# Kernel optimization log

Measured on AMD Instinct MI355X. Metric: run time of the kernel, lower is better.

The kernel has to match this reference:

```python
import jax, jax.numpy as jnp
import numpy as np

B, L, D, DFF, H, DK = 256, 193, 64, 256, 2, 32
EPS = 1e-5


def _ln(x, g, b):
    m = x.mean(-1, keepdims=True)
    v = ((x - m) ** 2).mean(-1, keepdims=True)
    return (x - m) / jnp.sqrt(v + EPS) * g + b


def setup_inputs() -> dict:
    key = jax.random.key(0)
    ks = jax.random.split(key, 20)
    inp = {}
    inp["state"] = jax.random.normal(ks[0], (B, L, D), jnp.float32)
    for i in range(6):
        inp[f"C{i+1}"] = jax.random.normal(ks[1 + i], (B, L, DFF), jnp.float32)
    s = 0.02
    # state Q/K/V projections (stored as [in, out]; y = x @ W + b)
    inp["Wq"] = jax.random.normal(ks[7], (D, D), jnp.float32) * s
    inp["Wk"] = jax.random.normal(ks[8], (D, D), jnp.float32) * s
    inp["Wv"] = jax.random.normal(ks[9], (D, D), jnp.float32) * s
    inp["bq"] = jnp.zeros((D,), jnp.float32)
    inp["bk"] = jnp.zeros((D,), jnp.float32)
    inp["bv"] = jnp.zeros((D,), jnp.float32)
    # context (C_cat, 6*dff=1536 -> 64) projections
    inp["WCq"] = jax.random.normal(ks[10], (6 * DFF, D), jnp.float32) * s
    inp["WCk"] = jax.random.normal(ks[11], (6 * DFF, D), jnp.float32) * s
    inp["WCv"] = jax.random.normal(ks[12], (6 * DFF, D), jnp.float32) * s
    inp["bCq"] = jnp.zeros((D,), jnp.float32)
    inp["bCk"] = jnp.zeros((D,), jnp.float32)
    inp["bCv"] = jnp.zeros((D,), jnp.float32)
    # LayerNorm params (6 QKV branch norms + norm1)
    for nm in ("QE", "KE", "VE", "QH", "KH", "VH", "1"):
        inp[f"g{nm}"] = jnp.ones((D,), jnp.float32)
        inp[f"be{nm}"] = jnp.zeros((D,), jnp.float32)
    # FFN
    inp["W1"] = jax.random.normal(ks[13], (D, 4 * D), jnp.float32) * s
    inp["bl1"] = jnp.zeros((4 * D,), jnp.float32)
    inp["W2"] = jax.random.normal(ks[14], (4 * D, D), jnp.float32) * s
    inp["bl2"] = jnp.zeros((D,), jnp.float32)
    return inp


def reference(state, C1, C2, C3, C4, C5, C6,
              Wq, Wk, Wv, bq, bk, bv,
              WCq, WCk, WCv, bCq, bCk, bCv,
              gQE, beQE, gKE, beKE, gVE, beVE,
              gQH, beQH, gKH, beKH, gVH, beVH,
              g1, be1, W1, bl1, W2, bl2):
    Ccat = jnp.concatenate([C1, C2, C3, C4, C5, C6], axis=-1)  # [B, L, 6*dff]
    # gated Q/K/V: LN(state proj) * LN(context proj)
    q = _ln(state @ Wq + bq, gQE, beQE) * _ln(Ccat @ WCq + bCq, gQH, beQH)
    k = _ln(state @ Wk + bk, gKE, beKE) * _ln(Ccat @ WCk + bCk, gKH, beKH)
    v = _ln(state @ Wv + bv, gVE, beVE) * _ln(Ccat @ WCv + bCv, gVH, beVH)
    q = q.reshape(B, L, H, DK).transpose(0, 2, 1, 3)  # [B, H, L, dk]
    k = k.reshape(B, L, H, DK).transpose(0, 2, 1, 3)
    v = v.reshape(B, L, H, DK).transpose(0, 2, 1, 3)
    scores = jnp.einsum("bhqd,bhkd->bhqk", q, k) / jnp.sqrt(jnp.float32(DK))
    attn = jax.nn.softmax(scores, axis=-1)
    out = jnp.einsum("bhqk,bhkd->bhqd", attn, v)
    attn_values = out.transpose(0, 2, 1, 3).reshape(B, L, H * DK)
    # dropout is identity in eval mode
    Z1 = state + attn_values
    Z2 = _ln(Z1, g1, be1)
    Z3 = jax.nn.gelu(Z2 @ W1 + bl1, approximate=False)
    Z4 = Z3 @ W2 + bl2
    Z5 = state + attn_values + Z4
    return Z5
```

## Files before the change

kernel.cpp:

```cpp
#include <hip/hip_runtime.h>
#include <math.h>

typedef unsigned short ushort_t;
typedef __attribute__((ext_vector_type(8))) short short8;
typedef __attribute__((ext_vector_type(4))) float floatx4;
typedef __attribute__((ext_vector_type(8))) unsigned short ushortx8;

#define NROW 49408
#define MT   772

__device__ __forceinline__ float b2f(ushort_t u){
  union { float f; unsigned int i; } v; v.i = ((unsigned int)u) << 16; return v.f;
}
__device__ __forceinline__ ushort_t f2b(float f){
  unsigned int i = __float_as_uint(f);
  unsigned int r = (i + 0x7FFFu + ((i >> 16) & 1u)) >> 16;
  return (ushort_t)r;
}

struct Args {
  const float *state,*C0,*C1,*C2,*C3,*C4,*C5;
  const float *Wq,*Wk,*Wv,*bq,*bk,*bv;
  const float *WCq,*WCk,*WCv,*bCq,*bCk,*bCv;
  const float *gQE,*beQE,*gKE,*beKE,*gVE,*beVE;
  const float *gQH,*beQH,*gKH,*beKH,*gVH,*beVH;
  const float *g1,*be1,*W1,*bl1,*W2,*bl2;
  float *qws,*kws,*vws;
  ushort_t *attws;
  ushort_t *weT,*whT,*w1T,*w2T;
  float *out;
};

__global__ __launch_bounds__(256) void k_prep(Args A){
  int i = blockIdx.x*256 + threadIdx.x;
  int stride = gridDim.x*256;
  const float* We[3] = {A.Wq, A.Wk, A.Wv};
  const float* Wh[3] = {A.WCq, A.WCk, A.WCv};
  for (int p=i; p<2*6144; p+=stride){
    int kc = p / 6144, r = p - kc*6144, n = r >> 5, kk = r & 31;
    A.weT[p] = f2b(We[n>>6][(kc*32+kk)*64 + (n&63)]);
  }
  for (int p=i; p<48*6144; p+=stride){
    int kc = p / 6144, r = p - kc*6144, n = r >> 5, kk = r & 31;
    A.whT[p] = f2b(Wh[n>>6][(kc*32+kk)*64 + (n&63)]);
  }
  for (int p=i; p<256*64; p+=stride){ int n=p>>6, k=p&63; A.w1T[p] = f2b(A.W1[k*256 + n]); }
  for (int p=i; p<64*256; p+=stride){ int n=p>>8, k=p&255; A.w2T[p] = f2b(A.W2[k*64 + n]); }
}

#define LDA 72
__global__ __launch_bounds__(256,2) void k_proj(Args A){
  const int mb = blockIdx.x;
  const int t  = threadIdx.x;
  const int w  = t >> 6;
  const int l  = t & 63;
  const int lr = l & 15;
  const int lq = l >> 4;
  const int arow = t >> 2, aseg = t & 3;

  struct __align__(16) SM {
    union {
      ushort_t Abuf[2][64*LDA];
      struct { float E[64][65]; float Hh[64][65]; } ln;
    };
  };
  __shared__ SM sm;

  floatx4 accH[3][4];
  floatx4 accE[3][4];
  #pragma unroll
  for (int jj=0;jj<3;jj++)
    #pragma unroll
    for (int ra=0;ra<4;ra++){ accH[jj][ra] = floatx4{0.f,0.f,0.f,0.f}; accE[jj][ra] = floatx4{0.f,0.f,0.f,0.f}; }

  auto loadA = [&](int k, float4* f){
    const float* src;
    if (k < 24){
      int sel = k >> 2;
      const float* cb = A.C0;
      if (sel==1) cb=A.C1; else if (sel==2) cb=A.C2; else if (sel==3) cb=A.C3;
      else if (sel==4) cb=A.C4; else if (sel==5) cb=A.C5;
      src = cb + (size_t)(mb*64 + arow)*256 + (k&3)*64 + aseg*16;
    } else {
      src = A.state + (size_t)(mb*64 + arow)*64 + aseg*16;
    }
    f[0] = ((const float4*)src)[0];
    f[1] = ((const float4*)src)[1];
    f[2] = ((const float4*)src)[2];
    f[3] = ((const float4*)src)[3];
  };
  auto loadB = [&](int k, short8* b){
    const ushort_t* bp = (k < 24) ? (A.whT + (size_t)(2*k)*6144) : A.weT;
    #pragma unroll
    for (int ks=0; ks<2; ++ks)
      #pragma unroll
      for (int jj=0; jj<3; ++jj)
        b[ks*3+jj] = *(const short8*)(bp + ks*6144 + (48*w + 16*jj + lr)*32 + lq*8);
  };
  auto storeA = [&](int buf, const float4* f){
    ushortx8 u0, u1;
    u0[0]=f2b(f[0].x); u0[1]=f2b(f[0].y); u0[2]=f2b(f[0].z); u0[3]=f2b(f[0].w);
    u0[4]=f2b(f[1].x); u0[5]=f2b(f[1].y); u0[6]=f2b(f[1].z); u0[7]=f2b(f[1].w);
    u1[0]=f2b(f[2].x); u1[1]=f2b(f[2].y); u1[2]=f2b(f[2].z); u1[3]=f2b(f[2].w);
    u1[4]=f2b(f[3].x); u1[5]=f2b(f[3].y); u1[6]=f2b(f[3].z); u1[7]=f2b(f[3].w);
    ushort_t* p = sm.Abuf[buf] + arow*LDA + aseg*16;
    *(ushortx8*)p = u0;
    *(ushortx8*)(p+8) = u1;
  };
  auto mfmaStep = [&](int cur, const short8* b, floatx4 (&acc)[3][4]){
    #pragma unroll
    for (int ks=0; ks<2; ++ks){
      short8 a[4];
      #pragma unroll
      for (int ra=0;ra<4;ra++)
        a[ra] = *(const short8*)(sm.Abuf[cur] + (16*ra + lr)*LDA + ks*32 + lq*8);
      #pragma unroll
      for (int jj=0;jj<3;jj++)
        #pragma unroll
        for (int ra=0;ra<4;ra++)
          acc[jj][ra] = __builtin_amdgcn_mfma_f32_16x16x32_bf16(a[ra], b[ks*3+jj], acc[jj][ra], 0,0,0);
    }
  };

  float4 rA[4], rB[4];
  short8 bA[6], bB[6];

  loadB(0, bA);
  loadA(0, rB);
  loadA(1, rA);
  storeA(0, rB);
  __syncthreads();

  for (int kc = 0; kc < 24; kc += 2){
    loadB(kc+1, bB);
    loadA(kc+2, rB);
    mfmaStep(0, bA, accH);
    storeA(1, rA);
    asm volatile("s_waitcnt lgkmcnt(0)" ::: "memory");
    __builtin_amdgcn_s_barrier();
    __builtin_amdgcn_sched_barrier(0);
    loadB(kc+2, bA);
    if (kc+3 <= 24) loadA(kc+3, rA);
    mfmaStep(1, bB, accH);
    storeA(0, rB);
    asm volatile("s_waitcnt lgkmcnt(0)" ::: "memory");
    __builtin_amdgcn_s_barrier();
    __builtin_amdgcn_sched_barrier(0);
  }
  mfmaStep(0, bA, accE);
  __syncthreads();

  const float* bEs[3]  = {A.bq,  A.bk,  A.bv};
  const float* bHs[3]  = {A.bCq, A.bCk, A.bCv};
  const float* gEs[3]  = {A.gQE, A.gKE, A.gVE};
  const float* beEs[3] = {A.beQE,A.beKE,A.beVE};
  const float* gHs[3]  = {A.gQH, A.gKH, A.gVH};
  const float* beHs[3] = {A.beQH,A.beKH,A.beVH};
  float* outw[3] = {A.qws, A.kws, A.vws};

  for (int g=0; g<3; ++g){
    #pragma unroll
    for (int jj=0;jj<3;jj++){
      int jg = 3*w + jj;
      if ((jg >> 2) == g){
        int colL = (jg & 3)*16 + lr;
        float be_ = bEs[g][colL];
        float bh_ = bHs[g][colL];
        #pragma unroll
        for (int ra=0;ra<4;ra++)
          #pragma unroll
          for (int r=0;r<4;r++){
            int row = 16*ra + lq*4 + r;
            sm.ln.E[row][colL]  = accE[jj][ra][r] + be_;
            sm.ln.Hh[row][colL] = accH[jj][ra][r] + bh_;
          }
      }
    }
    __syncthreads();
    {
      int r = t >> 2, q4 = t & 3;
      float sE=0.f, ssE=0.f, sH=0.f, ssH=0.f;
      #pragma unroll
      for (int c=0;c<16;c++){
        float e = sm.ln.E[r][q4*16+c];  sE += e; ssE += e*e;
        float h = sm.ln.Hh[r][q4*16+c]; sH += h; ssH += h*h;
      }
      sE  += __shfl_xor(sE,1);  sE  += __shfl_xor(sE,2);
      ssE += __shfl_xor(ssE,1); ssE += __shfl_xor(ssE,2);
      sH  += __shfl_xor(sH,1);  sH  += __shfl_xor(sH,2);
      ssH += __shfl_xor(ssH,1); ssH += __shfl_xor(ssH,2);
      float mE = sE*(1.f/64.f), vE = fmaxf(ssE*(1.f/64.f) - mE*mE, 0.f);
      float mH = sH*(1.f/64.f), vH = fmaxf(ssH*(1.f/64.f) - mH*mH, 0.f);
      float rE = rsqrtf(vE + 1e-5f), rH = rsqrtf(vH + 1e-5f);
      int G  = mb*64 + r;
      int bb = G / 193, lp = G - bb*193;
      float* ow = outw[g];
      #pragma unroll
      for (int c=0;c<16;c++){
        int cc = q4*16 + c;
        float e = (sm.ln.E[r][cc]-mE)*rE*gEs[g][cc] + beEs[g][cc];
        float h = (sm.ln.Hh[r][cc]-mH)*rH*gHs[g][cc] + beHs[g][cc];
        int hd = cc >> 5, d = cc & 31;
        ow[((size_t)(bb*2+hd)*193 + lp)*32 + d] = e*h;
      }
    }
    __syncthreads();
  }
}

__global__ __launch_bounds__(256) void k_attn(Args A){
  const int b = blockIdx.x, h = blockIdx.y;
  const int t = threadIdx.x;
  const size_t base = ((size_t)(b*2+h))*193*32;
  const float* __restrict__ kws = A.kws;
  const float* __restrict__ vws = A.vws;

  const int qrow = (t < 193) ? t : 192;
  float qreg[32], acc[32];
  {
    const float* qp = A.qws + base + qrow*32;
    #pragma unroll
    for (int d=0; d<32; d++){ qreg[d] = qp[d]; acc[d] = 0.f; }
  }
  float m = -1e30f, lsum = 0.f;
  for (int j=0; j<193; ++j){
    const float* kr = kws + base + j*32;
    const float* vr = vws + base + j*32;
    float s = 0.f;
    #pragma unroll
    for (int d=0; d<32; d++) s += qreg[d]*kr[d];
    s *= 0.17677669529663687f;
    float mn = fmaxf(m, s);
    float al = __expf(m - mn);
    float p  = __expf(s - mn);
    lsum = lsum*al + p;
    #pragma unroll
    for (int d=0; d<32; d++) acc[d] = acc[d]*al + p*vr[d];
    m = mn;
  }
  if (t < 193){
    float inv = 1.f/lsum;
    size_t G = (size_t)b*193 + t;
    #pragma unroll
    for (int d=0; d<32; d++) A.attws[G*64 + h*32 + d] = f2b(acc[d]*inv);
  }
}

#define LZ1 68
#define LZ2 72
#define LZ3 264
__global__ __launch_bounds__(256) void k_ffn(Args A){
  const int mb = blockIdx.x, t = threadIdx.x, w = t>>6, l = t&63, lr = l&15, lq = l>>4;
  __shared__ __align__(16) float    z1t[64*LZ1];
  __shared__ __align__(16) ushort_t z2t[64*LZ2];
  __shared__ __align__(16) ushort_t z3t[64*LZ3];

  {
    int row = t >> 2, seg = t & 3;
    const float* sp    = A.state + (size_t)(mb*64+row)*64 + seg*16;
    const ushort_t* ap = A.attws + (size_t)(mb*64+row)*64 + seg*16;
    float4 s0=((const float4*)sp)[0], s1=((const float4*)sp)[1],
           s2=((const float4*)sp)[2], s3=((const float4*)sp)[3];
    ushortx8 a0 = *(const ushortx8*)ap, a1 = *(const ushortx8*)(ap+8);
    float4 z0, z1, z2, z3;
    z0.x=s0.x+b2f(a0[0]); z0.y=s0.y+b2f(a0[1]); z0.z=s0.z+b2f(a0[2]); z0.w=s0.w+b2f(a0[3]);
    z1.x=s1.x+b2f(a0[4]); z1.y=s1.y+b2f(a0[5]); z1.z=s1.z+b2f(a0[6]); z1.w=s1.w+b2f(a0[7]);
    z2.x=s2.x+b2f(a1[0]); z2.y=s2.y+b2f(a1[1]); z2.z=s2.z+b2f(a1[2]); z2.w=s2.w+b2f(a1[3]);
    z3.x=s3.x+b2f(a1[4]); z3.y=s3.y+b2f(a1[5]); z3.z=s3.z+b2f(a1[6]); z3.w=s3.w+b2f(a1[7]);
    float* zp = z1t + row*LZ1 + seg*16;
    ((float4*)zp)[0]=z0; ((float4*)zp)[1]=z1; ((float4*)zp)[2]=z2; ((float4*)zp)[3]=z3;
  }
  __syncthreads();

  {
    int r = t >> 2, q4 = t & 3;
    float s=0.f, ss=0.f;
    #pragma unroll
    for (int c=0;c<16;c++){ float v = z1t[r*LZ1 + q4*16 + c]; s += v; ss += v*v; }
    s  += __shfl_xor(s,1);  s  += __shfl_xor(s,2);
    ss += __shfl_xor(ss,1); ss += __shfl_xor(ss,2);
    float mean = s*(1.f/64.f);
    float var  = fmaxf(ss*(1.f/64.f) - mean*mean, 0.f);
    float rstd = rsqrtf(var + 1e-5f);
    ushortx8 u0, u1;
    #pragma unroll
    for (int c=0;c<16;c++){
      int cc = q4*16 + c;
      float z2v = (z1t[r*LZ1 + cc]-mean)*rstd*A.g1[cc] + A.be1[cc];
      if (c < 8) u0[c] = f2b(z2v); else u1[c-8] = f2b(z2v);
    }
    ushort_t* zp = z2t + r*LZ2 + q4*16;
    *(ushortx8*)zp = u0;
    *(ushortx8*)(zp+8) = u1;
  }
  __syncthreads();

  floatx4 acc[4][4];
  #pragma unroll
  for (int jj=0;jj<4;jj++)
    #pragma unroll
    for (int ra=0;ra<4;ra++) acc[jj][ra] = floatx4{0.f,0.f,0.f,0.f};
  #pragma unroll
  for (int kc=0;kc<2;kc++){
    short8 a[4], b[4];
    #pragma unroll
    for (int ra=0;ra<4;ra++) a[ra] = *(const short8*)(z2t + (16*ra+lr)*LZ2 + kc*32 + lq*8);
    #pragma unroll
    for (int jj=0;jj<4;jj++) b[jj] = *(const short8*)(A.w1T + (size_t)(64*w + 16*jj + lr)*64 + kc*32 + lq*8);
    #pragma unroll
    for (int jj=0;jj<4;jj++)
      #pragma unroll
      for (int ra=0;ra<4;ra++)
        acc[jj][ra] = __builtin_amdgcn_mfma_f32_16x16x32_bf16(a[ra], b[jj], acc[jj][ra], 0,0,0);
  }
  #pragma unroll
  for (int jj=0;jj<4;jj++){
    int col = 64*w + 16*jj + lr;
    float bb = A.bl1[col];
    #pragma unroll
    for (int ra=0;ra<4;ra++)
      #pragma unroll
      for (int r=0;r<4;r++){
        int row = 16*ra + lq*4 + r;
        float x = acc[jj][ra][r] + bb;
        float gl = 0.5f*x*(1.0f + erff(x*0.70710678118654752f));
        z3t[row*LZ3 + col] = f2b(gl);
      }
  }
  __syncthreads();

  floatx4 o[4];
  #pragma unroll
  for (int ra=0;ra<4;ra++) o[ra] = floatx4{0.f,0.f,0.f,0.f};
  #pragma unroll
  for (int kc=0;kc<8;kc++){
    short8 a[4];
    short8 b = *(const short8*)(A.w2T + (size_t)(16*w + lr)*256 + kc*32 + lq*8);
    #pragma unroll
    for (int ra=0;ra<4;ra++) a[ra] = *(const short8*)(z3t + (16*ra+lr)*LZ3 + kc*32 + lq*8);
    #pragma unroll
    for (int ra=0;ra<4;ra++)
      o[ra] = __builtin_amdgcn_mfma_f32_16x16x32_bf16(a[ra], b, o[ra], 0,0,0);
  }
  int col = 16*w + lr;
  float bb = A.bl2[col];
  #pragma unroll
  for (int ra=0;ra<4;ra++)
    #pragma unroll
    for (int r=0;r<4;r++){
      int row = 16*ra + lq*4 + r;
      size_t idx = (size_t)(mb*64+row)*64 + col;
      A.out[idx] = o[ra][r] + bb + z1t[row*LZ1 + col];
    }
}

extern "C" void kernel_launch(void* const* d_in, const int* in_sizes, int n_in,
                              void* d_out, int out_size, void* d_ws, size_t ws_size,
                              hipStream_t stream){
  (void)in_sizes; (void)n_in; (void)out_size; (void)ws_size;
  Args A;
  A.state = (const float*)d_in[0];
  A.C0=(const float*)d_in[1]; A.C1=(const float*)d_in[2]; A.C2=(const float*)d_in[3];
  A.C3=(const float*)d_in[4]; A.C4=(const float*)d_in[5]; A.C5=(const float*)d_in[6];
  A.Wq=(const float*)d_in[7];  A.Wk=(const float*)d_in[8];  A.Wv=(const float*)d_in[9];
  A.bq=(const float*)d_in[10]; A.bk=(const float*)d_in[11]; A.bv=(const float*)d_in[12];
  A.WCq=(const float*)d_in[13]; A.WCk=(const float*)d_in[14]; A.WCv=(const float*)d_in[15];
  A.bCq=(const float*)d_in[16]; A.bCk=(const float*)d_in[17]; A.bCv=(const float*)d_in[18];
  A.gQE=(const float*)d_in[19]; A.beQE=(const float*)d_in[20];
  A.gKE=(const float*)d_in[21]; A.beKE=(const float*)d_in[22];
  A.gVE=(const float*)d_in[23]; A.beVE=(const float*)d_in[24];
  A.gQH=(const float*)d_in[25]; A.beQH=(const float*)d_in[26];
  A.gKH=(const float*)d_in[27]; A.beKH=(const float*)d_in[28];
  A.gVH=(const float*)d_in[29]; A.beVH=(const float*)d_in[30];
  A.g1=(const float*)d_in[31]; A.be1=(const float*)d_in[32];
  A.W1=(const float*)d_in[33]; A.bl1=(const float*)d_in[34];
  A.W2=(const float*)d_in[35]; A.bl2=(const float*)d_in[36];

  char* ws = (char*)d_ws;
  size_t off = 0;
  const size_t rowf = (size_t)NROW*64*sizeof(float);
  const size_t rowh = (size_t)NROW*64*2;
  A.qws  = (float*)(ws+off); off += rowf;
  A.kws  = (float*)(ws+off); off += rowf;
  A.vws  = (float*)(ws+off); off += rowf;
  A.attws= (ushort_t*)(ws+off); off += rowh;
  A.weT  = (ushort_t*)(ws+off); off += 192*64*2;
  A.whT  = (ushort_t*)(ws+off); off += (size_t)192*1536*2;
  A.w1T  = (ushort_t*)(ws+off); off += 256*64*2;
  A.w2T  = (ushort_t*)(ws+off); off += 64*256*2;
  A.out  = (float*)d_out;

  k_prep <<<dim3(256),    dim3(256), 0, stream>>>(A);
  k_proj <<<dim3(MT),     dim3(256), 0, stream>>>(A);
  k_attn <<<dim3(256,2),  dim3(256), 0, stream>>>(A);
  k_ffn  <<<dim3(MT),     dim3(256), 0, stream>>>(A);
}
```

Measured before the change: 636.8 us.

## Stage K/V in LDS and use lazy-rescale online softmax in attention kernel

Each attention block first copies its head's K and V tiles into shared memory, so the per-key loop reads LDS broadcasts instead of global memory. The query is pre-scaled by 1/sqrt(dk). The online softmax rescales the accumulator only when the running max grows by more than a threshold, which removes most per-key exp and scaling work. Output is written as packed 8-wide bf16 vectors. This costs about 49KB of LDS per block, which may limit occupancy, and the lazy rescale allows exponent values up to e^8 before renormalising.

```diff
diff --git a/kernel.cpp b/kernel.cpp
--- a/kernel.cpp
+++ b/kernel.cpp
@@ -212,37 +212,74 @@
   const int b = blockIdx.x, h = blockIdx.y;
   const int t = threadIdx.x;
   const size_t base = ((size_t)(b*2+h))*193*32;
-  const float* __restrict__ kws = A.kws;
-  const float* __restrict__ vws = A.vws;
+
+  __shared__ __align__(16) float Kl[193*32];
+  __shared__ __align__(16) float Vl[193*32];
+  {
+    const float4* ks = (const float4*)(A.kws + base);
+    const float4* vs = (const float4*)(A.vws + base);
+    float4* kd = (float4*)Kl;
+    float4* vd = (float4*)Vl;
+    for (int i = t; i < 1544; i += 256){ kd[i] = ks[i]; vd[i] = vs[i]; }
+  }
 
   const int qrow = (t < 193) ? t : 192;
-  float qreg[32], acc[32];
+  float4 qv[8], av[8];
   {
-    const float* qp = A.qws + base + qrow*32;
-    #pragma unroll
-    for (int d=0; d<32; d++){ qreg[d] = qp[d]; acc[d] = 0.f; }
-  }
+    const float4* qp = (const float4*)(A.qws + base + qrow*32);
+    #pragma unroll
+    for (int i=0;i<8;i++){
+      float4 q = qp[i];
+      const float sc = 0.17677669529663687f;
+      q.x*=sc; q.y*=sc; q.z*=sc; q.w*=sc;
+      qv[i] = q;
+      av[i] = float4{0.f,0.f,0.f,0.f};
+    }
+  }
+  __syncthreads();
+
   float m = -1e30f, lsum = 0.f;
+  #pragma unroll 2
   for (int j=0; j<193; ++j){
-    const float* kr = kws + base + j*32;
-    const float* vr = vws + base + j*32;
-    float s = 0.f;
-    #pragma unroll
-    for (int d=0; d<32; d++) s += qreg[d]*kr[d];
-    s *= 0.17677669529663687f;
-    float mn = fmaxf(m, s);
-    float al = __expf(m - mn);
-    float p  = __expf(s - mn);
-    lsum = lsum*al + p;
-    #pragma unroll
-    for (int d=0; d<32; d++) acc[d] = acc[d]*al + p*vr[d];
-    m = mn;
-  }
+    const float4* kr = (const float4*)(Kl + j*32);
+    float s0 = qv[0].x*kr[0].x + qv[0].y*kr[0].y + qv[0].z*kr[0].z + qv[0].w*kr[0].w;
+    float s1 = qv[1].x*kr[1].x + qv[1].y*kr[1].y + qv[1].z*kr[1].z + qv[1].w*kr[1].w;
+    float s2 = qv[2].x*kr[2].x + qv[2].y*kr[2].y + qv[2].z*kr[2].z + qv[2].w*kr[2].w;
+    float s3 = qv[3].x*kr[3].x + qv[3].y*kr[3].y + qv[3].z*kr[3].z + qv[3].w*kr[3].w;
+    s0 += qv[4].x*kr[4].x + qv[4].y*kr[4].y + qv[4].z*kr[4].z + qv[4].w*kr[4].w;
+    s1 += qv[5].x*kr[5].x + qv[5].y*kr[5].y + qv[5].z*kr[5].z + qv[5].w*kr[5].w;
+    s2 += qv[6].x*kr[6].x + qv[6].y*kr[6].y + qv[6].z*kr[6].z + qv[6].w*kr[6].w;
+    s3 += qv[7].x*kr[7].x + qv[7].y*kr[7].y + qv[7].z*kr[7].z + qv[7].w*kr[7].w;
+    float s = (s0+s1) + (s2+s3);
+    if (s > m + 8.f){
+      float al = __expf(m - s);
+      lsum *= al;
+      #pragma unroll
+      for (int i=0;i<8;i++){ av[i].x*=al; av[i].y*=al; av[i].z*=al; av[i].w*=al; }
+      m = s;
+    }
+    float p = __expf(s - m);
+    lsum += p;
+    const float4* vr = (const float4*)(Vl + j*32);
+    #pragma unroll
+    for (int i=0;i<8;i++){
+      av[i].x += p*vr[i].x; av[i].y += p*vr[i].y;
+      av[i].z += p*vr[i].z; av[i].w += p*vr[i].w;
+    }
+  }
+
   if (t < 193){
     float inv = 1.f/lsum;
     size_t G = (size_t)b*193 + t;
-    #pragma unroll
-    for (int d=0; d<32; d++) A.attws[G*64 + h*32 + d] = f2b(acc[d]*inv);
+    ushort_t* op = A.attws + G*64 + h*32;
+    #pragma unroll
+    for (int i=0;i<4;i++){
+      ushortx8 u;
+      float4 a0 = av[2*i], a1 = av[2*i+1];
+      u[0]=f2b(a0.x*inv); u[1]=f2b(a0.y*inv); u[2]=f2b(a0.z*inv); u[3]=f2b(a0.w*inv);
+      u[4]=f2b(a1.x*inv); u[5]=f2b(a1.y*inv); u[6]=f2b(a1.z*inv); u[7]=f2b(a1.w*inv);
+      *(ushortx8*)(op + i*8) = u;
+    }
   }
 }
 
```

New measurement: 523.0 us. 17.9% less time.
